# Optimization experiments

Measured on AMD Instinct MI355X. Metric: run time of the kernel, lower is better.

## Reference

```python
import jax, jax.numpy as jnp
import numpy as np

NUM_HEADS = 8   # input_dim: number of split chunks
HEAD_DIM = 10   # model_dim // num_heads; must be 10 to match Linear(10, 1)
MODEL_DIM = NUM_HEADS * HEAD_DIM
B, T = 64, 8192


def setup_inputs() -> dict:
    key = jax.random.key(0)
    k1, k2 = jax.random.split(key)
    x = jax.random.normal(k1, (B, T, MODEL_DIM), dtype=jnp.float32)
    w_proj = jax.random.normal(k2, (1, HEAD_DIM), dtype=jnp.float32) * 0.3
    b_proj = jnp.zeros((1,), dtype=jnp.float32)
    return {"x": x, "w_proj": w_proj, "b_proj": b_proj}


def reference(x, w_proj, b_proj):
    b, t, d = x.shape
    # split dim 2 into NUM_HEADS chunks of HEAD_DIM, stack on dim 0 -> [H,B,T,hd]
    q = x.reshape(b, t, NUM_HEADS, HEAD_DIM).transpose(2, 0, 1, 3)
    # key.transpose(-1,-2).sum(3).unsqueeze(2) == sum over T -> [H,B,1,hd]
    k_sum = q.sum(axis=2, keepdims=True)
    attn = jax.nn.softmax(jnp.tanh(q * k_sum / np.sqrt(HEAD_DIM).astype(np.float32)), axis=-1)
    t_out = attn * q                         # value == query == key == x splits
    v_q = t_out.sum(axis=2)                  # [H,B,hd]
    v_v = t_out.sum(axis=3).transpose(1, 0, 2)  # [B,H,T]
    # tiny Linear(hd=10 -> 1): gate [H,B,1]
    gate = jnp.tanh((v_q * v_q) @ w_proj.T + b_proj)
    # softmax over a size-1 axis is identically 1 (kept for faithfulness)
    gate = jax.nn.softmax(gate, axis=-1).transpose(1, 0, 2)  # [B,H,1]
    return v_v * gate                        # [B,H,T]
```

## Files before the change

### kernel.cpp

```cpp
#include <hip/hip_runtime.h>
#include <math.h>

#define BB 64
#define TT 8192
#define NH 8
#define HD 10
#define DD 80
#define NCHUNK 32
#define RSQRT10 0.31622776601683794f

__global__ __launch_bounds__(320) void ksum_kernel(const float* __restrict__ x,
                                                   float* __restrict__ gpart) {
    int chunk = blockIdx.x & (NCHUNK - 1);
    int b     = blockIdx.x >> 5;
    const float4* xp = (const float4*)(x + ((size_t)b * TT + (size_t)chunk * 256) * DD);

    int tid = threadIdx.x;
    int c4  = tid % 20;
    int r0  = tid / 20;

    float4 acc = make_float4(0.f, 0.f, 0.f, 0.f);
#pragma unroll
    for (int k = 0; k < 16; ++k) {
        float4 v = xp[(size_t)(r0 + k * 16) * 20 + c4];
        acc.x += v.x; acc.y += v.y; acc.z += v.z; acc.w += v.w;
    }

    __shared__ float red[320][4];
    red[tid][0] = acc.x; red[tid][1] = acc.y; red[tid][2] = acc.z; red[tid][3] = acc.w;
    __syncthreads();

    if (tid < DD) {
        int cc4 = tid >> 2, comp = tid & 3;
        float s = 0.f;
#pragma unroll
        for (int rr = 0; rr < 16; ++rr) s += red[cc4 + 20 * rr][comp];
        gpart[(b * NCHUNK + chunk) * DD + tid] = s;
    }
}

__global__ __launch_bounds__(256) void attn_kernel(const float* __restrict__ x,
                                                   const float* __restrict__ gpart,
                                                   float* __restrict__ out) {
    int chunk = blockIdx.x & 127;
    int b     = blockIdx.x >> 7;
    int t0    = chunk * 64;

    __shared__ float xs[64 * 81];
    __shared__ float ks[DD];

    const float4* xp = (const float4*)(x + ((size_t)b * TT + (size_t)t0) * DD);
    int tid = threadIdx.x;

#pragma unroll
    for (int k = 0; k < 5; ++k) {
        int f4  = tid + k * 256;
        float4 v = xp[f4];
        int row = f4 / 20;
        int col = (f4 % 20) * 4;
        float* dst = &xs[row * 81 + col];
        dst[0] = v.x; dst[1] = v.y; dst[2] = v.z; dst[3] = v.w;
    }
    if (tid < DD) {
        float s = 0.f;
#pragma unroll
        for (int c = 0; c < NCHUNK; ++c) s += gpart[(b * NCHUNK + c) * DD + tid];
        ks[tid] = s * RSQRT10;
    }
    __syncthreads();

    int g = tid >> 6;
    int r = tid & 63;
    int t = t0 + r;
    const float* qrow = &xs[r * 81 + g * 20];

#pragma unroll
    for (int hh = 0; hh < 2; ++hh) {
        int h = g * 2 + hh;
        float esum = 0.f, eq = 0.f;
#pragma unroll
        for (int d = 0; d < 10; ++d) {
            float q  = qrow[hh * 10 + d];
            float sv = q * ks[h * HD + d];
            float a  = fabsf(sv);
            float ex = __expf(-2.f * a);
            float th = copysignf((1.f - ex) * __builtin_amdgcn_rcpf(1.f + ex), sv);
            float e  = __expf(th);
            esum += e;
            eq   += e * q;
        }
        out[((size_t)(b * NH + h)) * TT + t] = eq * __builtin_amdgcn_rcpf(esum);
    }
}

extern "C" void kernel_launch(void* const* d_in, const int* in_sizes, int n_in,
                              void* d_out, int out_size, void* d_ws, size_t ws_size,
                              hipStream_t stream) {
    const float* x = (const float*)d_in[0];
    float* out   = (float*)d_out;
    float* gpart = (float*)d_ws;

    ksum_kernel<<<dim3(BB * NCHUNK), dim3(320), 0, stream>>>(x, gpart);
    attn_kernel<<<dim3(BB * (TT / 64)), dim3(256), 0, stream>>>(x, gpart, out);
}
```

Measured before the change: 262.6 us.

## Pre-reduce key sums in a separate kernel, fold exp2 scaling, vectorize LDS

Adds a small kernel that finishes the per-batch key-sum reduction once, so each of the 8192 attention blocks no longer re-reduces 32 partials from global memory. The 1/sqrt(10) and 2*log2(e) factors are folded into the key sum, so tanh and softmax are computed with native exp2 and FMA. The LDS tile stride becomes 84 so rows can be written and read as float4. This adds a third kernel launch and may raise LDS bank conflicts on the row-wise float4 reads.

```diff
diff --git a/kernel.cpp b/kernel.cpp
--- a/kernel.cpp
+++ b/kernel.cpp
@@ -7,7 +7,8 @@
 #define HD 10
 #define DD 80
 #define NCHUNK 32
-#define RSQRT10 0.31622776601683794f
+#define KSCALE 0.9123740929154171f
+#define LOG2E  1.4426950408889634f
 
 __global__ __launch_bounds__(320) void ksum_kernel(const float* __restrict__ x,
                                                    float* __restrict__ gpart) {
@@ -39,14 +40,27 @@
     }
 }
 
+__global__ __launch_bounds__(128) void ksfin_kernel(const float* __restrict__ gpart,
+                                                    float* __restrict__ ksf) {
+    int b = blockIdx.x;
+    int d = threadIdx.x;
+    if (d < DD) {
+        float s = 0.f;
+#pragma unroll
+        for (int c = 0; c < NCHUNK; ++c) s += gpart[(b * NCHUNK + c) * DD + d];
+        ksf[b * DD + d] = s * KSCALE;
+    }
+}
+
+#define XSTR 84
 __global__ __launch_bounds__(256) void attn_kernel(const float* __restrict__ x,
-                                                   const float* __restrict__ gpart,
+                                                   const float* __restrict__ ksf,
                                                    float* __restrict__ out) {
     int chunk = blockIdx.x & 127;
     int b     = blockIdx.x >> 7;
     int t0    = chunk * 64;
 
-    __shared__ float xs[64 * 81];
+    __shared__ float xs[64 * XSTR];
     __shared__ float ks[DD];
 
     const float4* xp = (const float4*)(x + ((size_t)b * TT + (size_t)t0) * DD);
@@ -55,24 +69,24 @@
 #pragma unroll
     for (int k = 0; k < 5; ++k) {
         int f4  = tid + k * 256;
-        float4 v = xp[f4];
         int row = f4 / 20;
-        int col = (f4 % 20) * 4;
-        float* dst = &xs[row * 81 + col];
-        dst[0] = v.x; dst[1] = v.y; dst[2] = v.z; dst[3] = v.w;
+        int col = f4 % 20;
+        *(float4*)&xs[row * XSTR + col * 4] = xp[f4];
     }
-    if (tid < DD) {
-        float s = 0.f;
-#pragma unroll
-        for (int c = 0; c < NCHUNK; ++c) s += gpart[(b * NCHUNK + c) * DD + tid];
-        ks[tid] = s * RSQRT10;
-    }
+    if (tid < DD) ks[tid] = ksf[b * DD + tid];
     __syncthreads();
 
     int g = tid >> 6;
     int r = tid & 63;
     int t = t0 + r;
-    const float* qrow = &xs[r * 81 + g * 20];
+
+    float q[20];
+    const float4* qrow = (const float4*)&xs[r * XSTR + g * 20];
+#pragma unroll
+    for (int k = 0; k < 5; ++k) {
+        float4 v = qrow[k];
+        q[4 * k] = v.x; q[4 * k + 1] = v.y; q[4 * k + 2] = v.z; q[4 * k + 3] = v.w;
+    }
 
 #pragma unroll
     for (int hh = 0; hh < 2; ++hh) {
@@ -80,14 +94,14 @@
         float esum = 0.f, eq = 0.f;
 #pragma unroll
         for (int d = 0; d < 10; ++d) {
-            float q  = qrow[hh * 10 + d];
-            float sv = q * ks[h * HD + d];
-            float a  = fabsf(sv);
-            float ex = __expf(-2.f * a);
-            float th = copysignf((1.f - ex) * __builtin_amdgcn_rcpf(1.f + ex), sv);
-            float e  = __expf(th);
+            float qv  = q[hh * 10 + d];
+            float sv  = qv * ks[h * HD + d];
+            float ex  = __builtin_amdgcn_exp2f(-fabsf(sv));
+            float num = __builtin_fmaf(-LOG2E, ex, LOG2E);
+            float tm  = num * __builtin_amdgcn_rcpf(1.f + ex);
+            float e   = __builtin_amdgcn_exp2f(copysignf(tm, sv));
             esum += e;
-            eq   += e * q;
+            eq    = __builtin_fmaf(e, qv, eq);
         }
         out[((size_t)(b * NH + h)) * TT + t] = eq * __builtin_amdgcn_rcpf(esum);
     }
@@ -99,7 +113,9 @@
     const float* x = (const float*)d_in[0];
     float* out   = (float*)d_out;
     float* gpart = (float*)d_ws;
+    float* ksf   = gpart + BB * NCHUNK * DD;
 
-    ksum_kernel<<<dim3(BB * NCHUNK), dim3(320), 0, stream>>>(x, gpart);
-    attn_kernel<<<dim3(BB * (TT / 64)), dim3(256), 0, stream>>>(x, gpart, out);
+    ksum_kernel <<<dim3(BB * NCHUNK), dim3(320), 0, stream>>>(x, gpart);
+    ksfin_kernel<<<dim3(BB),          dim3(128), 0, stream>>>(gpart, ksf);
+    attn_kernel <<<dim3(BB * (TT/64)), dim3(256), 0, stream>>>(x, ksf, out);
 }
```

Measured after the change: 263.3 us. Within noise of the previous version (+0.2%).
